# Kernel tuning notes

Hardware: AMD Instinct MI355X
Metric: run time of the kernel (lower is better)

Reference implementation:

```python
import jax, jax.numpy as jnp
import numpy as np

DIN = 1024
DIM = 1024
NUM_HEADS = 16
HEAD_DIM = DIM // NUM_HEADS
SEQ_LEN = 2048
BATCH = 2


def setup_inputs() -> dict:
    key = jax.random.key(0)
    ks = jax.random.split(key, 5)
    s = 0.02
    x = jax.random.normal(ks[0], (BATCH, SEQ_LEN, DIN), dtype=jnp.float32)
    # torch nn.Linear weights are (out_features, in_features)
    wq = jax.random.normal(ks[1], (DIM, DIN), dtype=jnp.float32) * s
    wk = jax.random.normal(ks[2], (DIM, DIN), dtype=jnp.float32) * s
    wv = jax.random.normal(ks[3], (DIM, DIN), dtype=jnp.float32) * s
    wo = jax.random.normal(ks[4], (DIM, DIM), dtype=jnp.float32) * s
    return {"x": x, "wq": wq, "wk": wk, "wv": wv, "wo": wo}


def reference(x, wq, wk, wv, wo):
    bs, seq_len, _ = x.shape
    # project and split heads: [b, h, s, d]
    def split(z):
        return z.reshape(bs, seq_len, NUM_HEADS, HEAD_DIM).transpose(0, 2, 1, 3)
    q = split(x @ wq.T)
    k = split(x @ wk.T)
    v = split(x @ wv.T)
    # raw scores, causal mask applied BEFORE the 1/sqrt(d) scaling (as in source;
    # -inf is invariant to positive scaling so math matches standard causal attn)
    att = jnp.einsum('bhqd,bhkd->bhqk', q, k)
    causal = jnp.triu(jnp.ones((seq_len, seq_len), dtype=bool), k=1)
    att = jnp.where(causal, -jnp.inf, att)
    att = jax.nn.softmax(att / jnp.sqrt(jnp.float32(HEAD_DIM)), axis=-1)
    ctx = jnp.einsum('bhqk,bhkd->bhqd', att, v)
    ctx = ctx.transpose(0, 2, 1, 3).reshape(bs, seq_len, DIM)
    return ctx @ wo.T
```

## Files before the change

kernel.cpp:

```cpp
#include <hip/hip_runtime.h>
#include <stdint.h>

#define DIN 1024
#define DIMM 1024
#define NH 16
#define HD 64
#define SEQ 2048
#define BATCH 2
#define MTOT (BATCH*SEQ)
#define SCALE 0.125f

typedef __bf16 bf16;
typedef __bf16 bf16x8 __attribute__((ext_vector_type(8)));
typedef __bf16 bf16x4 __attribute__((ext_vector_type(4)));
typedef float f32x4 __attribute__((ext_vector_type(4)));

__device__ __forceinline__ void async16(bf16* lds, const bf16* g) {
  __builtin_amdgcn_global_load_lds(
      (const __attribute__((address_space(1))) void*)g,
      (__attribute__((address_space(3))) void*)lds, 16, 0, 0);
}

__global__ __launch_bounds__(256) void convert_all(const float* __restrict__ x,
                                                   const float* __restrict__ wq,
                                                   const float* __restrict__ wk,
                                                   const float* __restrict__ wv,
                                                   const float* __restrict__ wo,
                                                   bf16* __restrict__ xb,
                                                   bf16* __restrict__ Wb) {
  const int t = blockIdx.x * 256 + threadIdx.x;
#pragma unroll
  for (int i = 0; i < 4; ++i) {
    const int c = t + i * 262144;
    const float* src;
    bf16* dst;
    if (c < 524288) {
      src = x + (size_t)c * 8;
      dst = xb + (size_t)c * 8;
    } else {
      const int cw = c - 524288;
      const int w = cw >> 17;
      const int off = (cw & 131071) * 8;
      const float* wp = (w == 0) ? wq : (w == 1) ? wk : (w == 2) ? wv : wo;
      src = wp + off;
      dst = Wb + (size_t)w * 1048576 + off;
    }
    f32x4 a = *(const f32x4*)src;
    f32x4 b = *(const f32x4*)(src + 4);
    bf16x8 r;
    r[0] = (bf16)a[0]; r[1] = (bf16)a[1]; r[2] = (bf16)a[2]; r[3] = (bf16)a[3];
    r[4] = (bf16)b[0]; r[5] = (bf16)b[1]; r[6] = (bf16)b[2]; r[7] = (bf16)b[3];
    *(bf16x8*)dst = r;
  }
}

__device__ __forceinline__ void mm128_core(const bf16* __restrict__ A,
                                           const bf16* __restrict__ B,
                                           int K, int mbase, int nbase,
                                           bf16* As, bf16* Bs,
                                           f32x4 acc[4][4]) {
  const int tid  = threadIdx.x;
  const int lane = tid & 63;
  const int wave = tid >> 6;
  const int lrow = lane & 15;
  const int quad = lane >> 4;
  const int wr = (wave >> 1) * 64;
  const int wc = (wave & 1) * 64;
  const int srow = tid >> 3;
  const int scol = (tid & 7) * 8;
  const int sx   = (((tid & 7) ^ (srow & 7))) * 8;

  for (int k0 = 0; k0 < K; k0 += 64) {
#pragma unroll
    for (int i = 0; i < 4; ++i) {
      async16(&As[(i * 32 + srow) * 64 + scol],
              &A[(size_t)(mbase + i * 32 + srow) * K + k0 + sx]);
      async16(&Bs[(i * 32 + srow) * 64 + scol],
              &B[(size_t)(nbase + i * 32 + srow) * K + k0 + sx]);
    }
    __syncthreads();
#pragma unroll
    for (int h = 0; h < 2; ++h) {
      const int cx = ((h * 4 + quad) ^ (lrow & 7)) * 8;
      bf16x8 af[4], bfr[4];
#pragma unroll
      for (int i = 0; i < 4; ++i) {
        af[i]  = *(const bf16x8*)&As[(wr + i * 16 + lrow) * 64 + cx];
        bfr[i] = *(const bf16x8*)&Bs[(wc + i * 16 + lrow) * 64 + cx];
      }
#pragma unroll
      for (int mt = 0; mt < 4; ++mt)
#pragma unroll
        for (int nt = 0; nt < 4; ++nt)
          acc[mt][nt] = __builtin_amdgcn_mfma_f32_16x16x32_bf16(af[mt], bfr[nt], acc[mt][nt], 0, 0, 0);
    }
    __syncthreads();
  }
}

__global__ __launch_bounds__(256) void qkv_gemm(const bf16* __restrict__ A,
                                                const bf16* __restrict__ B,
                                                bf16* __restrict__ Q,
                                                bf16* __restrict__ Kb,
                                                bf16* __restrict__ Vt) {
  __shared__ bf16 As[128 * 64];
  __shared__ bf16 Bs[128 * 64];
  const int lane = threadIdx.x & 63;
  const int wave = threadIdx.x >> 6;
  const int lrow = lane & 15;
  const int quad = lane >> 4;
  const int wr = (wave >> 1) * 64;
  const int wc = (wave & 1) * 64;
  const int lin = blockIdx.x;
  const int xcd = lin & 7;
  const int idx = lin >> 3;
  const int nbase = (xcd * 3 + idx % 3) * 128;
  const int mbase = (idx / 3) * 128;

  f32x4 acc[4][4] = {};
  mm128_core(A, B, DIN, mbase, nbase, As, Bs, acc);

#pragma unroll
  for (int mt = 0; mt < 4; ++mt) {
    const int m0 = mbase + wr + mt * 16 + quad * 4;
#pragma unroll
    for (int nt = 0; nt < 4; ++nt) {
      const int n16 = nbase + wc + nt * 16;
      const int n = n16 + lrow;
      if (n16 < 1024) {
#pragma unroll
        for (int rr = 0; rr < 4; ++rr)
          Q[(size_t)(m0 + rr) * 1024 + n] = (bf16)acc[mt][nt][rr];
      } else if (n16 < 2048) {
#pragma unroll
        for (int rr = 0; rr < 4; ++rr)
          Kb[(size_t)(m0 + rr) * 1024 + (n - 1024)] = (bf16)acc[mt][nt][rr];
      } else {
        const int nn = n - 2048;
        const int row = ((m0 >> 11) * 16 + (nn >> 6)) * 64 + (nn & 63);
        bf16x4 ov;
#pragma unroll
        for (int rr = 0; rr < 4; ++rr) ov[rr] = (bf16)acc[mt][nt][rr];
        *(bf16x4*)&Vt[(size_t)row * SEQ + (m0 & 2047)] = ov;
      }
    }
  }
}

__global__ __launch_bounds__(256) void proj_gemm(const bf16* __restrict__ A,
                                                 const bf16* __restrict__ B,
                                                 float* __restrict__ C) {
  __shared__ bf16 As[128 * 64];
  __shared__ bf16 Bs[64 * 64];
  const int tid  = threadIdx.x;
  const int lane = tid & 63;
  const int wave = tid >> 6;
  const int lrow = lane & 15;
  const int quad = lane >> 4;
  const int wr = (wave >> 1) * 64;
  const int wc = (wave & 1) * 32;
  const int lin = blockIdx.x;
  const int xcd = lin & 7;
  const int idx = lin >> 3;
  const int nbase = (xcd * 2 + (idx & 1)) * 64;
  const int mbase = (idx >> 1) * 128;
  const int srow = tid >> 3;
  const int scol = (tid & 7) * 8;
  const int sx   = ((tid & 7) ^ (srow & 7)) * 8;

  f32x4 acc[4][2] = {};

  for (int k0 = 0; k0 < DIMM; k0 += 64) {
#pragma unroll
    for (int i = 0; i < 4; ++i)
      async16(&As[(i * 32 + srow) * 64 + scol],
              &A[(size_t)(mbase + i * 32 + srow) * DIMM + k0 + sx]);
#pragma unroll
    for (int i = 0; i < 2; ++i)
      async16(&Bs[(i * 32 + srow) * 64 + scol],
              &B[(size_t)(nbase + i * 32 + srow) * DIMM + k0 + sx]);
    __syncthreads();
#pragma unroll
    for (int h = 0; h < 2; ++h) {
      const int cx = ((h * 4 + quad) ^ (lrow & 7)) * 8;
      bf16x8 af[4], bfr[2];
#pragma unroll
      for (int i = 0; i < 4; ++i)
        af[i] = *(const bf16x8*)&As[(wr + i * 16 + lrow) * 64 + cx];
#pragma unroll
      for (int i = 0; i < 2; ++i)
        bfr[i] = *(const bf16x8*)&Bs[(wc + i * 16 + lrow) * 64 + cx];
#pragma unroll
      for (int mt = 0; mt < 4; ++mt)
#pragma unroll
        for (int nt = 0; nt < 2; ++nt)
          acc[mt][nt] = __builtin_amdgcn_mfma_f32_16x16x32_bf16(af[mt], bfr[nt], acc[mt][nt], 0, 0, 0);
    }
    __syncthreads();
  }

#pragma unroll
  for (int mt = 0; mt < 4; ++mt) {
    const int m0 = mbase + wr + mt * 16 + quad * 4;
#pragma unroll
    for (int nt = 0; nt < 2; ++nt) {
      const int n = nbase + wc + nt * 16 + lrow;
#pragma unroll
      for (int rr = 0; rr < 4; ++rr)
        C[(size_t)(m0 + rr) * 1024 + n] = acc[mt][nt][rr];
    }
  }
}

__global__ __launch_bounds__(256, 5) void attn(const bf16* __restrict__ Q,
                                               const bf16* __restrict__ K,
                                               const bf16* __restrict__ Vt,
                                               bf16* __restrict__ O) {
  __shared__ bf16 Ks[2][64 * 64];
  __shared__ bf16 Vts[2][64 * 64];
  const int tid  = threadIdx.x;
  const int wave = tid >> 6;
  const int lane = tid & 63;
  const int lrow = lane & 15;
  const int quad = lane >> 4;
  const int lin  = blockIdx.x;
  const int bh   = lin & 31;
  const int j    = lin >> 5;
  const int t    = j & 7;
  const int grp  = j >> 3;
  const int qi   = (grp == 0) ? (31 - t) : (grp == 1) ? t
                 : (grp == 2) ? (23 - t) : (8 + t);
  const int b = bh >> 4;
  const int h = bh & 15;
  const int qw = qi * 64 + wave * 16;
  const int ntiles = qi + 1;

  const bf16* Qh  = Q  + (size_t)(b * SEQ) * DIMM + h * HD;
  const bf16* Kh  = K  + (size_t)(b * SEQ) * DIMM + h * HD;
  const bf16* Vth = Vt + (size_t)bh * 64 * SEQ;

  const int srow = tid >> 3;
  const int sdst = srow * 64 + (tid & 7) * 8;
  const int sx   = ((tid & 7) ^ (srow & 7)) * 8;
  const int cx0 = ((0 + quad) ^ (lrow & 7)) * 8;
  const int cx1 = ((4 + quad) ^ (lrow & 7)) * 8;
  const int LL = lrow & 7;
  const int qh = quad >> 1, ql = quad & 1;
  int vc[4];
#pragma unroll
  for (int g = 0; g < 4; ++g)
    vc[g] = ((((2 * g + qh) ^ LL) << 1) | ql) * 4;

  bf16x8 qf0 = *(const bf16x8*)&Qh[(size_t)(qw + lrow) * DIMM + quad * 8];
  bf16x8 qf1 = *(const bf16x8*)&Qh[(size_t)(qw + lrow) * DIMM + 32 + quad * 8];

  const bf16* kg0 = Kh + (size_t)srow * DIMM + sx;
  const bf16* kg1 = kg0 + (size_t)32 * DIMM;
  const bf16* vg0 = Vth + (size_t)srow * SEQ + sx;
  const bf16* vg1 = vg0 + (size_t)32 * SEQ;

  async16(&Ks[0][sdst],         kg0);
  async16(&Ks[0][sdst + 2048],  kg1);
  async16(&Vts[0][sdst],        vg0);
  async16(&Vts[0][sdst + 2048], vg1);
  __syncthreads();

  float lsum = 0.f;
  f32x4 o_acc[4] = {};
  int cur = 0;
  const float C1 = 0.18033688f;

  for (int kt = 0; kt < ntiles; ++kt) {
    if (kt + 1 < ntiles) {
      kg0 += 64 * DIMM; kg1 += 64 * DIMM; vg0 += 64; vg1 += 64;
      bf16* Kn = Ks[cur ^ 1];
      bf16* Vn = Vts[cur ^ 1];
      async16(&Kn[sdst],        kg0);
      async16(&Kn[sdst + 2048], kg1);
      async16(&Vn[sdst],        vg0);
      async16(&Vn[sdst + 2048], vg1);
    }
    const bf16* Kc = Ks[cur];
    const bf16* Vc = Vts[cur];
    f32x4 s[4] = {};
#pragma unroll
    for (int gg = 0; gg < 4; ++gg) {
      bf16x8 kf0 = *(const bf16x8*)&Kc[(gg * 16 + lrow) * 64 + cx0];
      bf16x8 kf1 = *(const bf16x8*)&Kc[(gg * 16 + lrow) * 64 + cx1];
      s[gg] = __builtin_amdgcn_mfma_f32_16x16x32_bf16(kf0, qf0, s[gg], 0, 0, 0);
      s[gg] = __builtin_amdgcn_mfma_f32_16x16x32_bf16(kf1, qf1, s[gg], 0, 0, 0);
    }
    if (kt == qi) {
      const int qrow = qw + lrow;
      const int kbase = kt * 64;
#pragma unroll
      for (int gg = 0; gg < 4; ++gg)
#pragma unroll
        for (int r = 0; r < 4; ++r)
          s[gg][r] = (kbase + gg * 16 + quad * 4 + r > qrow) ? -1e30f : s[gg][r];
    }
    bf16x8 pf0, pf1;
#pragma unroll
    for (int gg = 0; gg < 4; ++gg)
#pragma unroll
      for (int r = 0; r < 4; ++r) {
        const float p = __builtin_amdgcn_exp2f(s[gg][r] * C1);
        lsum += p;
        if (gg < 2) pf0[(gg & 1) * 4 + r] = (bf16)p;
        else        pf1[(gg & 1) * 4 + r] = (bf16)p;
      }
#pragma unroll
    for (int dt = 0; dt < 4; ++dt) {
      const bf16* Vr = &Vc[(dt * 16 + lrow) * 64];
      bf16x4 a0 = *(const bf16x4*)&Vr[vc[0]];
      bf16x4 a1 = *(const bf16x4*)&Vr[vc[1]];
      bf16x4 b0 = *(const bf16x4*)&Vr[vc[2]];
      bf16x4 b1 = *(const bf16x4*)&Vr[vc[3]];
      bf16x8 vfA = __builtin_shufflevector(a0, a1, 0, 1, 2, 3, 4, 5, 6, 7);
      bf16x8 vfB = __builtin_shufflevector(b0, b1, 0, 1, 2, 3, 4, 5, 6, 7);
      o_acc[dt] = __builtin_amdgcn_mfma_f32_16x16x32_bf16(vfA, pf0, o_acc[dt], 0, 0, 0);
      o_acc[dt] = __builtin_amdgcn_mfma_f32_16x16x32_bf16(vfB, pf1, o_acc[dt], 0, 0, 0);
    }
    __syncthreads();
    cur ^= 1;
  }

  lsum += __shfl_xor(lsum, 16);
  lsum += __shfl_xor(lsum, 32);
  const float rl = __builtin_amdgcn_rcpf(lsum);
  bf16* Ob = O + (size_t)(b * SEQ + qw + lrow) * DIMM + h * HD;
#pragma unroll
  for (int dt = 0; dt < 4; ++dt) {
    bf16x4 ov;
#pragma unroll
    for (int r = 0; r < 4; ++r)
      ov[r] = (bf16)(o_acc[dt][r] * rl);
    *(bf16x4*)&Ob[dt * 16 + quad * 4] = ov;
  }
}

extern "C" void kernel_launch(void* const* d_in, const int* in_sizes, int n_in,
                              void* d_out, int out_size, void* d_ws, size_t ws_size,
                              hipStream_t stream) {
  const float* x  = (const float*)d_in[0];
  const float* wq = (const float*)d_in[1];
  const float* wk = (const float*)d_in[2];
  const float* wv = (const float*)d_in[3];
  const float* wo = (const float*)d_in[4];

  const size_t M4 = (size_t)MTOT * DIMM;
  bf16* xb  = (bf16*)d_ws;
  bf16* Wb  = xb + M4;
  bf16* Q   = Wb + M4;
  bf16* Kb  = Q + M4;
  bf16* Vt  = Kb + M4;
  bf16* CTX = xb;
  float* out = (float*)d_out;

  convert_all<<<dim3(1024), dim3(256), 0, stream>>>(x, wq, wk, wv, wo, xb, Wb);
  qkv_gemm<<<dim3(768), dim3(256), 0, stream>>>(xb, Wb, Q, Kb, Vt);
  attn<<<dim3(BATCH * NH * (SEQ / 64)), dim3(256), 0, stream>>>(Q, Kb, Vt, CTX);
  proj_gemm<<<dim3(512), dim3(256), 0, stream>>>(CTX, Wb + 3 * 1048576, out);
}
```

Measured before the change: 178.0 us.

## Double-buffer QKV GEMM with larger 256x192 tiles and 8 waves

Rewrites the QKV projection GEMM to use 512-thread blocks computing 256x192 output tiles, 64x96 per wave. LDS is double-buffered so the async global-to-LDS load of the next K slice is issued before computing the current one. This gives one sync per K step instead of two and more reuse per loaded tile. In exchange it uses much more LDS per block, so only one block fits per CU. The grid drops to 256 blocks, which leaves little room to hide tail imbalance.

Result: faster. 169.5 us (-4.8%).

```diff
diff --git a/kernel.cpp b/kernel.cpp
--- a/kernel.cpp
+++ b/kernel.cpp
@@ -54,78 +54,86 @@
   }
 }
 
-__device__ __forceinline__ void mm128_core(const bf16* __restrict__ A,
-                                           const bf16* __restrict__ B,
-                                           int K, int mbase, int nbase,
-                                           bf16* As, bf16* Bs,
-                                           f32x4 acc[4][4]) {
+__global__ __launch_bounds__(512, 2) void qkv_gemm(const bf16* __restrict__ A,
+                                                   const bf16* __restrict__ B,
+                                                   bf16* __restrict__ Q,
+                                                   bf16* __restrict__ Kb,
+                                                   bf16* __restrict__ Vt) {
+  __shared__ bf16 As[2][256 * 64];
+  __shared__ bf16 Bs[2][192 * 64];
   const int tid  = threadIdx.x;
   const int lane = tid & 63;
   const int wave = tid >> 6;
   const int lrow = lane & 15;
   const int quad = lane >> 4;
-  const int wr = (wave >> 1) * 64;
-  const int wc = (wave & 1) * 64;
+  const int wrow = wave >> 1;
+  const int wcol = wave & 1;
+  const int lin  = blockIdx.x;
+  const int xcd  = lin & 7;
+  const int idx  = lin >> 3;
+  const int nbase = (xcd * 2 + (idx & 1)) * 192;
+  const int mbase = (idx >> 1) * 256;
+
   const int srow = tid >> 3;
-  const int scol = (tid & 7) * 8;
-  const int sx   = (((tid & 7) ^ (srow & 7))) * 8;
-
-  for (int k0 = 0; k0 < K; k0 += 64) {
-#pragma unroll
-    for (int i = 0; i < 4; ++i) {
-      async16(&As[(i * 32 + srow) * 64 + scol],
-              &A[(size_t)(mbase + i * 32 + srow) * K + k0 + sx]);
-      async16(&Bs[(i * 32 + srow) * 64 + scol],
-              &B[(size_t)(nbase + i * 32 + srow) * K + k0 + sx]);
-    }
+  const int sdst = srow * 64 + (tid & 7) * 8;
+  const int sx   = ((tid & 7) ^ (srow & 7)) * 8;
+
+  const bf16* ap = A + (size_t)(mbase + srow) * DIN + sx;
+  const bf16* bp = B + (size_t)(nbase + srow) * DIN + sx;
+
+  f32x4 acc[4][6] = {};
+
+#define QKV_STAGE(bufi)                                            \
+  do {                                                             \
+    _Pragma("unroll")                                              \
+    for (int i = 0; i < 4; ++i)                                    \
+      async16(&As[bufi][sdst + i * 4096], ap + (size_t)i * 64 * DIN); \
+    _Pragma("unroll")                                              \
+    for (int i = 0; i < 3; ++i)                                    \
+      async16(&Bs[bufi][sdst + i * 4096], bp + (size_t)i * 64 * DIN); \
+  } while (0)
+
+#define QKV_COMPUTE(bufi)                                          \
+  do {                                                             \
+    _Pragma("unroll")                                              \
+    for (int h = 0; h < 2; ++h) {                                  \
+      const int cx = ((h * 4 + quad) ^ (lrow & 7)) * 8;            \
+      bf16x8 af[4], bfr[6];                                        \
+      _Pragma("unroll")                                            \
+      for (int i = 0; i < 4; ++i)                                  \
+        af[i] = *(const bf16x8*)&As[bufi][(wrow * 64 + i * 16 + lrow) * 64 + cx]; \
+      _Pragma("unroll")                                            \
+      for (int j = 0; j < 6; ++j)                                  \
+        bfr[j] = *(const bf16x8*)&Bs[bufi][(wcol * 96 + j * 16 + lrow) * 64 + cx]; \
+      _Pragma("unroll")                                            \
+      for (int i = 0; i < 4; ++i)                                  \
+        _Pragma("unroll")                                          \
+        for (int j = 0; j < 6; ++j)                                \
+          acc[i][j] = __builtin_amdgcn_mfma_f32_16x16x32_bf16(af[i], bfr[j], acc[i][j], 0, 0, 0); \
+    }                                                              \
+  } while (0)
+
+  QKV_STAGE(0);
+  __syncthreads();
+  int cur = 0;
+  for (int t = 0; t < 15; ++t) {
+    ap += 64; bp += 64;
+    QKV_STAGE(cur ^ 1);
+    QKV_COMPUTE(cur);
     __syncthreads();
-#pragma unroll
-    for (int h = 0; h < 2; ++h) {
-      const int cx = ((h * 4 + quad) ^ (lrow & 7)) * 8;
-      bf16x8 af[4], bfr[4];
-#pragma unroll
-      for (int i = 0; i < 4; ++i) {
-        af[i]  = *(const bf16x8*)&As[(wr + i * 16 + lrow) * 64 + cx];
-        bfr[i] = *(const bf16x8*)&Bs[(wc + i * 16 + lrow) * 64 + cx];
-      }
-#pragma unroll
-      for (int mt = 0; mt < 4; ++mt)
-#pragma unroll
-        for (int nt = 0; nt < 4; ++nt)
-          acc[mt][nt] = __builtin_amdgcn_mfma_f32_16x16x32_bf16(af[mt], bfr[nt], acc[mt][nt], 0, 0, 0);
-    }
-    __syncthreads();
-  }
-}
-
-__global__ __launch_bounds__(256) void qkv_gemm(const bf16* __restrict__ A,
-                                                const bf16* __restrict__ B,
-                                                bf16* __restrict__ Q,
-                                                bf16* __restrict__ Kb,
-                                                bf16* __restrict__ Vt) {
-  __shared__ bf16 As[128 * 64];
-  __shared__ bf16 Bs[128 * 64];
-  const int lane = threadIdx.x & 63;
-  const int wave = threadIdx.x >> 6;
-  const int lrow = lane & 15;
-  const int quad = lane >> 4;
-  const int wr = (wave >> 1) * 64;
-  const int wc = (wave & 1) * 64;
-  const int lin = blockIdx.x;
-  const int xcd = lin & 7;
-  const int idx = lin >> 3;
-  const int nbase = (xcd * 3 + idx % 3) * 128;
-  const int mbase = (idx / 3) * 128;
-
-  f32x4 acc[4][4] = {};
-  mm128_core(A, B, DIN, mbase, nbase, As, Bs, acc);
+    cur ^= 1;
+  }
+  QKV_COMPUTE(cur);
+
+#undef QKV_STAGE
+#undef QKV_COMPUTE
 
 #pragma unroll
   for (int mt = 0; mt < 4; ++mt) {
-    const int m0 = mbase + wr + mt * 16 + quad * 4;
-#pragma unroll
-    for (int nt = 0; nt < 4; ++nt) {
-      const int n16 = nbase + wc + nt * 16;
+    const int m0 = mbase + wrow * 64 + mt * 16 + quad * 4;
+#pragma unroll
+    for (int nt = 0; nt < 6; ++nt) {
+      const int n16 = nbase + wcol * 96 + nt * 16;
       const int n = n16 + lrow;
       if (n16 < 1024) {
 #pragma unroll
@@ -358,7 +366,7 @@
   float* out = (float*)d_out;
 
   convert_all<<<dim3(1024), dim3(256), 0, stream>>>(x, wq, wk, wv, wo, xb, Wb);
-  qkv_gemm<<<dim3(768), dim3(256), 0, stream>>>(xb, Wb, Q, Kb, Vt);
+  qkv_gemm<<<dim3(256), dim3(512), 0, stream>>>(xb, Wb, Q, Kb, Vt);
   attn<<<dim3(BATCH * NH * (SEQ / 64)), dim3(256), 0, stream>>>(Q, Kb, Vt, CTX);
   proj_gemm<<<dim3(512), dim3(256), 0, stream>>>(CTX, Wb + 3 * 1048576, out);
 }
```
